# Kernel optimization log

Measured on AMD Instinct MI355X. Metric: run time of the kernel, lower is better.

## Reference

```python
import jax, jax.numpy as jnp
import numpy as np

EPS = 1e-5  # nn.LayerNorm default
H = 16      # n_heads

def _ln(x, s, b):
    m = x.mean(-1, keepdims=True)
    v = x.var(-1, keepdims=True)
    return (x - m) / jnp.sqrt(v + EPS) * s + b


def setup_inputs() -> dict:
    key = jax.random.key(0)
    B, T, D, L, V = 2, 1024, 1024, 6, 32000
    ks = jax.random.split(key, 10)
    def n(k, shape):
        return jax.random.normal(k, shape, dtype=jnp.float32) * 0.02
    return dict(
        x=jax.random.randint(ks[0], (B, T), 0, V),
        tok_emb=n(ks[1], (V, D)),
        pos_emb=n(ks[2], (T, D)),
        Wq=n(ks[3], (L, D, D)), bq=jnp.zeros((L, D), jnp.float32),
        Wk=n(ks[4], (L, D, D)), bk=jnp.zeros((L, D), jnp.float32),
        Wv=n(ks[5], (L, D, D)), bv=jnp.zeros((L, D), jnp.float32),
        ln1_s=jnp.ones((L, D), jnp.float32), ln1_b=jnp.zeros((L, D), jnp.float32),
        W1=n(ks[6], (L, D, 4 * D)), b1=jnp.zeros((L, 4 * D), jnp.float32),
        W2=n(ks[7], (L, 4 * D, D)), b2=jnp.zeros((L, D), jnp.float32),
        ln2_s=jnp.ones((L, D), jnp.float32), ln2_b=jnp.zeros((L, D), jnp.float32),
        Wout=n(ks[8], (D, V)), bout=jnp.zeros((V,), jnp.float32),
    )


def reference(x, tok_emb, pos_emb, Wq, bq, Wk, bk, Wv, bv, ln1_s, ln1_b,
              W1, b1, W2, b2, ln2_s, ln2_b, Wout, bout):
    B, T = x.shape
    D = tok_emb.shape[1]
    hd = D // H
    # embeddings (dropout = identity in eval)
    h = tok_emb[x] + pos_emb[:T]
    # additive causal mask: +1.0 on allowed (tril ones kept), -inf elsewhere,
    # exactly matching torch's tril-ones masked_fill mask
    tril = jnp.tril(jnp.ones((T, T), dtype=h.dtype))
    mask = jnp.where(tril == 0, -jnp.inf, 1.0).astype(h.dtype)
    scale = jnp.asarray(1.0 / np.sqrt(hd), h.dtype)

    def block(h, p):
        wq, bq_, wk, bk_, wv, bv_, l1s, l1b, w1, b1_, w2, b2_, l2s, l2b = p
        def heads(W, b):  # [B,T,D] -> [B,H,T,hd]
            return (h @ W + b).reshape(B, T, H, hd).transpose(0, 2, 1, 3)
        q, k, v = heads(wq, bq_), heads(wk, bk_), heads(wv, bv_)
        s = jnp.einsum('bhqd,bhkd->bhqk', q, k) * scale + mask
        a = jax.nn.softmax(s, axis=-1)
        o = jnp.einsum('bhqk,bhkd->bhqd', a, v).transpose(0, 2, 1, 3).reshape(B, T, D)
        hi = _ln(o + h, l1s, l1b)
        f = jax.nn.relu(hi @ w1 + b1_) @ w2 + b2_
        return _ln(f + hi, l2s, l2b), None

    h, _ = jax.lax.scan(block, h, (Wq, bq, Wk, bk, Wv, bv, ln1_s, ln1_b,
                                   W1, b1, W2, b2, ln2_s, ln2_b))
    return h @ Wout + bout
```

## Files before the change

kernel.cpp:

```cpp
#include <hip/hip_runtime.h>
#include <cstdint>
#include <cstddef>

typedef short bf16x8 __attribute__((ext_vector_type(8)));
typedef float f32x4 __attribute__((ext_vector_type(4)));
typedef unsigned short us4 __attribute__((ext_vector_type(4)));

#define DEV static __device__ __forceinline__

DEV unsigned short f2bf(float f) {
  union { float f; unsigned u; } v; v.f = f;
  unsigned r = v.u + 0x7FFFu + ((v.u >> 16) & 1u);
  return (unsigned short)(r >> 16);
}

DEV void gll16(const void* g, void* l) {
  __builtin_amdgcn_global_load_lds((const __attribute__((address_space(1))) void*)g,
                                   (__attribute__((address_space(3))) void*)l,
                                   16, 0, 0);
}

DEV void embed_body(const int* __restrict__ x, const float* __restrict__ te,
                    const float* __restrict__ pe, float* __restrict__ hf,
                    unsigned short* __restrict__ hb, int row, int tid) {
  int t = row & 1023;
  int tok = x[row];
  float4 v = ((const float4*)(te + (size_t)tok * 1024))[tid];
  float4 p = ((const float4*)(pe + (size_t)t * 1024))[tid];
  v.x += p.x; v.y += p.y; v.z += p.z; v.w += p.w;
  ((float4*)(hf + (size_t)row * 1024))[tid] = v;
  us4 bv; bv[0] = f2bf(v.x); bv[1] = f2bf(v.y); bv[2] = f2bf(v.z); bv[3] = f2bf(v.w);
  ((us4*)(hb + (size_t)row * 1024))[tid] = bv;
}

DEV void wconv_body(const float* __restrict__ W, unsigned short* __restrict__ Wt,
                    int K, int N, int b, float (*tile)[33], int tid) {
  const int nb = N >> 5;
  const int n0 = (b % nb) * 32, k0 = (b / nb) * 32;
  const int tx = tid & 31, ty = tid >> 5;
#pragma unroll
  for (int i = 0; i < 4; ++i)
    tile[ty * 4 + i][tx] = W[(size_t)(k0 + ty * 4 + i) * N + n0 + tx];
  __syncthreads();
#pragma unroll
  for (int i = 0; i < 4; ++i)
    Wt[(size_t)(n0 + ty * 4 + i) * K + k0 + tx] = f2bf(tile[tx][ty * 4 + i]);
}

template <int NP>
DEV void ln_body(const float* __restrict__ a1, const float* __restrict__ res,
                 const float* __restrict__ s, const float* __restrict__ bb,
                 float* __restrict__ out_f, unsigned short* __restrict__ out_b,
                 int row, int tid, float* red) {
  float4 x = ((const float4*)(a1 + (size_t)row * 1024))[tid];
  float4 rv = ((const float4*)(res + (size_t)row * 1024))[tid];
  x.x += rv.x; x.y += rv.y; x.z += rv.z; x.w += rv.w;
#pragma unroll
  for (int pimg = 1; pimg < NP; ++pimg) {
    float4 x2 = ((const float4*)(a1 + (size_t)pimg * 2097152 + (size_t)row * 1024))[tid];
    x.x += x2.x; x.y += x2.y; x.z += x2.z; x.w += x2.w;
  }
  float sum = x.x + x.y + x.z + x.w;
  float sq = x.x * x.x + x.y * x.y + x.z * x.z + x.w * x.w;
#pragma unroll
  for (int mm = 1; mm < 64; mm <<= 1) {
    sum += __shfl_xor(sum, mm, 64);
    sq += __shfl_xor(sq, mm, 64);
  }
  int wid = tid >> 6, lane = tid & 63;
  if (lane == 0) { red[wid] = sum; red[4 + wid] = sq; }
  __syncthreads();
  sum = red[0] + red[1] + red[2] + red[3];
  sq = red[4] + red[5] + red[6] + red[7];
  float mean = sum * (1.f / 1024.f);
  float var = sq * (1.f / 1024.f) - mean * mean;
  float rstd = rsqrtf(var + 1e-5f);
  float4 sv = ((const float4*)s)[tid];
  float4 bv = ((const float4*)bb)[tid];
  float4 y;
  y.x = (x.x - mean) * rstd * sv.x + bv.x;
  y.y = (x.y - mean) * rstd * sv.y + bv.y;
  y.z = (x.z - mean) * rstd * sv.z + bv.z;
  y.w = (x.w - mean) * rstd * sv.w + bv.w;
  ((float4*)(out_f + (size_t)row * 1024))[tid] = y;
  us4 ob; ob[0] = f2bf(y.x); ob[1] = f2bf(y.y); ob[2] = f2bf(y.z); ob[3] = f2bf(y.w);
  ((us4*)(out_b + (size_t)row * 1024))[tid] = ob;
}

DEV void wconv5_select(int bid, const float* Wqf, const float* Wkf,
                       const float* Wvf, const float* W1f, const float* W2f,
                       unsigned short* wsc, float (*tile)[33], int tid) {
  const float* W; unsigned short* Wt; int K, N, b;
  if (bid < 3072) {
    const int sgl = bid >> 10; b = bid & 1023;
    W = sgl == 0 ? Wqf : (sgl == 1 ? Wkf : Wvf);
    Wt = wsc + (size_t)sgl * 1048576; K = 1024; N = 1024;
  } else if (bid < 7168) {
    b = bid - 3072; W = W1f; Wt = wsc + 3145728; K = 1024; N = 4096;
  } else {
    b = bid - 7168; W = W2f; Wt = wsc + 7340032; K = 4096; N = 1024;
  }
  wconv_body(W, Wt, K, N, b, tile, tid);
}

__global__ __launch_bounds__(256) void embed_wconv_kernel(
    const int* __restrict__ x, const float* __restrict__ te,
    const float* __restrict__ pe, float* __restrict__ hf,
    unsigned short* __restrict__ hb,
    const float* __restrict__ Wqf, const float* __restrict__ Wkf,
    const float* __restrict__ Wvf, const float* __restrict__ W1f,
    const float* __restrict__ W2f, unsigned short* __restrict__ wsc) {
  __shared__ float tile[32][33];
  const int bid = blockIdx.x;
  if (bid < 2048) {
    embed_body(x, te, pe, hf, hb, bid, threadIdx.x);
    return;
  }
  wconv5_select(bid - 2048, Wqf, Wkf, Wvf, W1f, W2f, wsc, tile, threadIdx.x);
}

template <int NP>
__global__ __launch_bounds__(256) void ln_wconv5_kernel(
    const float* __restrict__ a1, const float* __restrict__ res,
    const float* __restrict__ s, const float* __restrict__ bb,
    float* __restrict__ out_f, unsigned short* __restrict__ out_b,
    const float* __restrict__ Wqf, const float* __restrict__ Wkf,
    const float* __restrict__ Wvf, const float* __restrict__ W1f,
    const float* __restrict__ W2f, unsigned short* __restrict__ wsc) {
  __shared__ float tile[32][33];
  __shared__ float red[8];
  const int bid = blockIdx.x;
  if (bid < 2048) {
    ln_body<NP>(a1, res, s, bb, out_f, out_b, bid, threadIdx.x, red);
    return;
  }
  wconv5_select(bid - 2048, Wqf, Wkf, Wvf, W1f, W2f, wsc, tile, threadIdx.x);
}

template <int NP>
__global__ __launch_bounds__(256) void ln_add_kernel(
    const float* __restrict__ a1, const float* __restrict__ res,
    const float* __restrict__ s, const float* __restrict__ bb,
    float* __restrict__ out_f, unsigned short* __restrict__ out_b) {
  __shared__ float red[8];
  ln_body<NP>(a1, res, s, bb, out_f, out_b, blockIdx.x, threadIdx.x, red);
}

__global__ __launch_bounds__(256) void wconv_kernel(
    const float* __restrict__ W, unsigned short* __restrict__ Wt, int K, int N) {
  __shared__ float tile[32][33];
  const int nb = N >> 5;
  wconv_body(W, Wt, K, N, blockIdx.y * nb + blockIdx.x, tile, threadIdx.x);
}

template <int BM, int EPI>
__global__ __launch_bounds__(512) void gemm5_kernel(
    const unsigned short* __restrict__ A, const unsigned short* __restrict__ Bt,
    const float* __restrict__ bias1, const float* __restrict__ bias2,
    const float* __restrict__ bias3, void* __restrict__ C1,
    void* __restrict__ C2, void* __restrict__ C3,
    int M, int N, int Kstride, int klen, int nbm) {
  constexpr int BN = 128, BK = 64;
  constexpr int MFR = BM / 64;
  constexpr int AIT = BM / 64;
  __shared__ unsigned short lA[BM * BK];
  __shared__ unsigned short lB[BN * BK];
  const int tid = threadIdx.x;
  const int wid = tid >> 6, lane = tid & 63;
  const int g = lane >> 4, c = lane & 15;
  const int wm = wid >> 1, wn = wid & 1;

  const int nwg = gridDim.x;
  const int q = nwg >> 3, r = nwg & 7;
  const int xcd = blockIdx.x & 7, jj = blockIdx.x >> 3;
  const int wgid = (xcd < r) ? (xcd * (q + 1) + jj)
                             : (r * (q + 1) + (xcd - r) * q + jj);
  const int bm = (wgid % nbm) * BM;
  const int bn = (wgid / nbm) * BN;
  const int k0 = blockIdx.z * klen;

  f32x4 acc[MFR][4];
#pragma unroll
  for (int mi = 0; mi < MFR; ++mi)
#pragma unroll
    for (int ni = 0; ni < 4; ++ni) acc[mi][ni] = f32x4{0.f, 0.f, 0.f, 0.f};

  for (int kb = 0; kb < klen; kb += BK) {
#pragma unroll
    for (int it = 0; it < AIT; ++it) {
      int chunk = it * 512 + tid;
      int row = chunk >> 3, cr = chunk & 7;
      int sc = cr ^ (row & 7);
      gll16(A + (size_t)(bm + row) * Kstride + k0 + kb + sc * 8,
            lA + (size_t)(it * 512 + wid * 64) * 8);
    }
#pragma unroll
    for (int it = 0; it < 2; ++it) {
      int chunk = it * 512 + tid;
      int row = chunk >> 3, cr = chunk & 7;
      int sc = cr ^ (row & 7);
      gll16(Bt + (size_t)(bn + row) * Kstride + k0 + kb + sc * 8,
            lB + (size_t)(it * 512 + wid * 64) * 8);
    }
    __syncthreads();
#pragma unroll
    for (int kk = 0; kk < 2; ++kk) {
      bf16x8 af[MFR], bfr[4];
#pragma unroll
      for (int mi = 0; mi < MFR; ++mi) {
        int row = wm * (BM / 4) + mi * 16 + c;
        int ch = (kk * 4 + g) ^ (row & 7);
        af[mi] = *(const bf16x8*)(lA + row * BK + ch * 8);
      }
#pragma unroll
      for (int ni = 0; ni < 4; ++ni) {
        int row = wn * 64 + ni * 16 + c;
        int ch = (kk * 4 + g) ^ (row & 7);
        bfr[ni] = *(const bf16x8*)(lB + row * BK + ch * 8);
      }
#pragma unroll
      for (int mi = 0; mi < MFR; ++mi)
#pragma unroll
        for (int ni = 0; ni < 4; ++ni)
          acc[mi][ni] = __builtin_amdgcn_mfma_f32_16x16x32_bf16(
              af[mi], bfr[ni], acc[mi][ni], 0, 0, 0);
    }
    __syncthreads();
  }

  const bool z0 = (blockIdx.z == 0);
#pragma unroll
  for (int mi = 0; mi < MFR; ++mi) {
    const int row0 = bm + wm * (BM / 4) + mi * 16 + g * 4;
#pragma unroll
    for (int ni = 0; ni < 4; ++ni) {
      const int col = bn + wn * 64 + ni * 16 + c;
      if constexpr (EPI == 0) {
        float* C = (float*)C1 + (size_t)blockIdx.z * M * N;
        const float bv = z0 ? bias1[col] : 0.f;
#pragma unroll
        for (int rr = 0; rr < 4; ++rr)
          C[(size_t)(row0 + rr) * N + col] = acc[mi][ni][rr] + bv;
      } else if constexpr (EPI == 2) {
        const float bv = bias1[col];
#pragma unroll
        for (int rr = 0; rr < 4; ++rr)
          ((unsigned short*)C1)[(size_t)(row0 + rr) * N + col] =
              f2bf(fmaxf(acc[mi][ni][rr] + bv, 0.f));
      } else {
        if (col < 1024) {
          const float bv = bias1[col];
#pragma unroll
          for (int rr = 0; rr < 4; ++rr)
            ((unsigned short*)C1)[(size_t)(row0 + rr) * 1024 + col] =
                f2bf(acc[mi][ni][rr] + bv);
        } else if (col < 2048) {
          const float bv = bias2[col - 1024];
#pragma unroll
          for (int rr = 0; rr < 4; ++rr)
            ((unsigned short*)C2)[(size_t)(row0 + rr) * 1024 + (col - 1024)] =
                f2bf(acc[mi][ni][rr] + bv);
        } else {
          const int cp = col - 2048;
          const float bv = bias3[cp];
          const int hh = cp >> 6, hd = cp & 63;
#pragma unroll
          for (int rr = 0; rr < 4; ++rr) {
            const int row = row0 + rr;
            const int b = row >> 10, t = row & 1023;
            ((unsigned short*)C3)[(size_t)((b * 16 + hh) * 64 + hd) * 1024 + t] =
                f2bf(acc[mi][ni][rr] + bv);
          }
        }
      }
    }
  }
}

__global__ __launch_bounds__(256) void attn_kernel(
    const unsigned short* __restrict__ q, const unsigned short* __restrict__ k,
    const unsigned short* __restrict__ vt, float* __restrict__ o) {
  __shared__ unsigned short lK[128 * 64];
  __shared__ unsigned short lV[64 * 128];
  __shared__ unsigned short lP[4][16 * 128];
  const int tid = threadIdx.x, wid = tid >> 6, lane = tid & 63;
  const int g = lane >> 4, c = lane & 15;
  const int qb = blockIdx.x * 64;
  const int h = blockIdx.y;
  const int b = blockIdx.z;
  const int qw = qb + wid * 16;

  bf16x8 aq[2];
#pragma unroll
  for (int kk = 0; kk < 2; ++kk)
    aq[kk] = *(const bf16x8*)(q + (size_t)(b * 1024 + qw + c) * 1024 + h * 64 + kk * 32 + g * 8);

  float m_run[4], l_run[4];
  f32x4 acc_o[4];
#pragma unroll
  for (int rr = 0; rr < 4; ++rr) { m_run[rr] = -INFINITY; l_run[rr] = 0.f; }
#pragma unroll
  for (int ni = 0; ni < 4; ++ni) acc_o[ni] = f32x4{0.f, 0.f, 0.f, 0.f};

  const int ntiles = (qb >> 7) + 1;
  for (int kt = 0; kt < ntiles; ++kt) {
#pragma unroll
    for (int it = 0; it < 4; ++it) {
      int chunk = it * 256 + tid;
      int row = chunk >> 3, cr = chunk & 7;
      int sc = cr ^ (row & 7);
      gll16(k + (size_t)(b * 1024 + kt * 128 + row) * 1024 + h * 64 + sc * 8,
            lK + (size_t)(it * 256 + wid * 64) * 8);
    }
#pragma unroll
    for (int it = 0; it < 4; ++it) {
      int chunk = it * 256 + tid;
      int row = chunk >> 4, cr = chunk & 15;
      int sc = cr ^ (row & 7);
      gll16(vt + (size_t)((b * 16 + h) * 64 + row) * 1024 + kt * 128 + sc * 8,
            lV + (size_t)(it * 256 + wid * 64) * 8);
    }
    __syncthreads();

    f32x4 accs[8];
#pragma unroll
    for (int ni = 0; ni < 8; ++ni) accs[ni] = f32x4{0.f, 0.f, 0.f, 0.f};
    __builtin_amdgcn_s_setprio(1);
#pragma unroll
    for (int kk = 0; kk < 2; ++kk)
#pragma unroll
      for (int ni = 0; ni < 8; ++ni) {
        int row = ni * 16 + c;
        int ch = (kk * 4 + g) ^ (row & 7);
        bf16x8 kf = *(const bf16x8*)(lK + row * 64 + ch * 8);
        accs[ni] = __builtin_amdgcn_mfma_f32_16x16x32_bf16(aq[kk], kf, accs[ni], 0, 0, 0);
      }
    __builtin_amdgcn_s_setprio(0);

    const bool diag = (kt == ntiles - 1);
    float p[8][4], rowmax[4];
#pragma unroll
    for (int rr = 0; rr < 4; ++rr) rowmax[rr] = -INFINITY;
#pragma unroll
    for (int ni = 0; ni < 8; ++ni)
#pragma unroll
      for (int rr = 0; rr < 4; ++rr) {
        float s = accs[ni][rr] * 0.125f;
        if (diag) {
          int ktok = kt * 128 + ni * 16 + c;
          int qtok = qw + g * 4 + rr;
          if (ktok > qtok) s = -INFINITY;
        }
        p[ni][rr] = s;
        rowmax[rr] = fmaxf(rowmax[rr], s);
      }
#pragma unroll
    for (int mm = 1; mm < 16; mm <<= 1)
#pragma unroll
      for (int rr = 0; rr < 4; ++rr)
        rowmax[rr] = fmaxf(rowmax[rr], __shfl_xor(rowmax[rr], mm, 64));

    float alpha[4];
#pragma unroll
    for (int rr = 0; rr < 4; ++rr) {
      float mn = fmaxf(m_run[rr], rowmax[rr]);
      alpha[rr] = __expf(m_run[rr] - mn);
      m_run[rr] = mn;
    }
#pragma unroll
    for (int ni = 0; ni < 8; ++ni)
#pragma unroll
      for (int rr = 0; rr < 4; ++rr) p[ni][rr] = __expf(p[ni][rr] - m_run[rr]);

    float rowsum[4];
#pragma unroll
    for (int rr = 0; rr < 4; ++rr)
      rowsum[rr] = ((p[0][rr] + p[1][rr]) + (p[2][rr] + p[3][rr])) +
                   ((p[4][rr] + p[5][rr]) + (p[6][rr] + p[7][rr]));
#pragma unroll
    for (int mm = 1; mm < 16; mm <<= 1)
#pragma unroll
      for (int rr = 0; rr < 4; ++rr) rowsum[rr] += __shfl_xor(rowsum[rr], mm, 64);
#pragma unroll
    for (int rr = 0; rr < 4; ++rr) l_run[rr] = l_run[rr] * alpha[rr] + rowsum[rr];
#pragma unroll
    for (int ni = 0; ni < 4; ++ni)
#pragma unroll
      for (int rr = 0; rr < 4; ++rr) acc_o[ni][rr] *= alpha[rr];

#pragma unroll
    for (int ni = 0; ni < 8; ++ni)
#pragma unroll
      for (int rr = 0; rr < 4; ++rr) {
        int qrow = g * 4 + rr;
        int tok = ni * 16 + c;
        int ch = (tok >> 3) ^ (qrow & 7);
        lP[wid][qrow * 128 + ch * 8 + (tok & 7)] = f2bf(p[ni][rr]);
      }

    __builtin_amdgcn_s_setprio(1);
#pragma unroll
    for (int kk = 0; kk < 4; ++kk) {
      int kc = kk * 4 + g;
      int chp = kc ^ (c & 7);
      bf16x8 pa = *(const bf16x8*)(&lP[wid][c * 128 + chp * 8]);
#pragma unroll
      for (int ni = 0; ni < 4; ++ni) {
        int row = ni * 16 + c;
        int ch = kc ^ (row & 7);
        bf16x8 vf = *(const bf16x8*)(lV + row * 128 + ch * 8);
        acc_o[ni] = __builtin_amdgcn_mfma_f32_16x16x32_bf16(pa, vf, acc_o[ni], 0, 0, 0);
      }
    }
    __builtin_amdgcn_s_setprio(0);
    __syncthreads();
  }

#pragma unroll
  for (int ni = 0; ni < 4; ++ni)
#pragma unroll
    for (int rr = 0; rr < 4; ++rr) {
      int row = b * 1024 + qw + g * 4 + rr;
      int col = h * 64 + ni * 16 + c;
      o[(size_t)row * 1024 + col] = acc_o[ni][rr] / l_run[rr];
    }
}

extern "C" void kernel_launch(void* const* d_in, const int* in_sizes, int n_in,
                              void* d_out, int out_size, void* d_ws, size_t ws_size,
                              hipStream_t stream) {
  const int D = 1024, DFF = 4096, V = 32000, L = 6;
  const int* x = (const int*)d_in[0];
  const float* tok_emb = (const float*)d_in[1];
  const float* pos_emb = (const float*)d_in[2];
  const float* Wq = (const float*)d_in[3];  const float* bq = (const float*)d_in[4];
  const float* Wk = (const float*)d_in[5];  const float* bk = (const float*)d_in[6];
  const float* Wv = (const float*)d_in[7];  const float* bv = (const float*)d_in[8];
  const float* ln1s = (const float*)d_in[9];  const float* ln1b = (const float*)d_in[10];
  const float* W1 = (const float*)d_in[11];  const float* b1 = (const float*)d_in[12];
  const float* W2 = (const float*)d_in[13];  const float* b2 = (const float*)d_in[14];
  const float* ln2s = (const float*)d_in[15]; const float* ln2b = (const float*)d_in[16];
  const float* Wout = (const float*)d_in[17]; const float* bout = (const float*)d_in[18];

  char* ws = (char*)d_ws;
  float* h_res = (float*)(ws + 0);
  float* hi_res = (float*)(ws + 8388608);
  float* tmp = (float*)(ws + 16777216);
  unsigned short* hbf = (unsigned short*)(ws + 25165824);
  unsigned short* qb_ = (unsigned short*)(ws + 29360128);
  unsigned short* kb_ = (unsigned short*)(ws + 33554432);
  unsigned short* vtb = (unsigned short*)(ws + 37748736);
  unsigned short* ffn1 = (unsigned short*)(ws + 41943040);
  unsigned short* wsc = (unsigned short*)(ws + 58720256);
  float* part = (float*)(ws + 58720256 + 25165824);

  embed_wconv_kernel<<<13312, 256, 0, stream>>>(
      x, tok_emb, pos_emb, h_res, hbf,
      Wq, Wk, Wv, W1, W2, wsc);

  for (int l = 0; l < L; ++l) {
    gemm5_kernel<128, 4><<<384, 512, 0, stream>>>(
        hbf, wsc, bq + l * D, bk + l * D, bv + l * D, qb_, kb_, vtb,
        2048, 3072, D, D, 16);
    attn_kernel<<<dim3(16, 16, 2), 256, 0, stream>>>(qb_, kb_, vtb, tmp);
    ln_add_kernel<1><<<2048, 256, 0, stream>>>(
        tmp, h_res, ln1s + l * D, ln1b + l * D, hi_res, hbf);
    gemm5_kernel<256, 2><<<256, 512, 0, stream>>>(
        hbf, wsc + 3145728, b1 + l * DFF, nullptr, nullptr, ffn1, nullptr, nullptr,
        2048, DFF, D, D, 8);
    gemm5_kernel<256, 0><<<dim3(64, 1, 4), 512, 0, stream>>>(
        ffn1, wsc + 7340032, b2 + l * D, nullptr, nullptr, part, nullptr, nullptr,
        2048, D, DFF, 1024, 8);
    if (l < L - 1) {
      ln_wconv5_kernel<4><<<13312, 256, 0, stream>>>(
          part, hi_res, ln2s + l * D, ln2b + l * D, h_res, hbf,
          Wq + (size_t)(l + 1) * D * D, Wk + (size_t)(l + 1) * D * D,
          Wv + (size_t)(l + 1) * D * D, W1 + (size_t)(l + 1) * D * DFF,
          W2 + (size_t)(l + 1) * DFF * D, wsc);
    } else {
      ln_add_kernel<4><<<2048, 256, 0, stream>>>(
          part, hi_res, ln2s + l * D, ln2b + l * D, h_res, hbf);
    }
  }

  wconv_kernel<<<dim3(1000, 32), 256, 0, stream>>>(Wout, wsc, D, V);
  gemm5_kernel<256, 0><<<2000, 512, 0, stream>>>(
      hbf, wsc, bout, nullptr, nullptr, (float*)d_out, nullptr, nullptr,
      2048, V, D, D, 8);
}
```

Baseline: 1.084 ms.

## Add double-buffered FFN1 GEMM and widen attention blocks to 128 queries

Adds a new FFN1 GEMM kernel that double-buffers A and B tiles in LDS, issuing the next K-tile's global-to-LDS loads while MFMAs run on the current tile, with one barrier per iteration. Separately, the attention kernel goes to 512 threads and 128 query rows per block, so each K/V tile loaded into LDS is shared by eight waves instead of four. The GEMM doubles its LDS footprint, which can lower occupancy. The larger attention blocks halve the grid and make causal load imbalance between blocks worse.

```diff
diff --git a/kernel.cpp b/kernel.cpp
--- a/kernel.cpp
+++ b/kernel.cpp
@@ -19,6 +19,8 @@
                                    (__attribute__((address_space(3))) void*)l,
                                    16, 0, 0);
 }
+
+DEV void vm0() { asm volatile("s_waitcnt vmcnt(0)" ::: "memory"); }
 
 DEV void embed_body(const int* __restrict__ x, const float* __restrict__ te,
                     const float* __restrict__ pe, float* __restrict__ hf,
@@ -277,15 +279,114 @@
   }
 }
 
-__global__ __launch_bounds__(256) void attn_kernel(
+template <int EPI>
+__global__ __launch_bounds__(512) void gemm5d_kernel(
+    const unsigned short* __restrict__ A, const unsigned short* __restrict__ Bt,
+    const float* __restrict__ bias1, void* __restrict__ C1,
+    int M, int N, int Kstride, int klen, int nbm) {
+  constexpr int BM = 256, BN = 128, BK = 64;
+  __shared__ unsigned short lA[2][BM * BK];
+  __shared__ unsigned short lB[2][BN * BK];
+  const int tid = threadIdx.x;
+  const int wid = tid >> 6, lane = tid & 63;
+  const int g = lane >> 4, c = lane & 15;
+  const int wm = wid >> 1, wn = wid & 1;
+
+  const int nwg = gridDim.x;
+  const int q = nwg >> 3, r = nwg & 7;
+  const int xcd = blockIdx.x & 7, jj = blockIdx.x >> 3;
+  const int wgid = (xcd < r) ? (xcd * (q + 1) + jj)
+                             : (r * (q + 1) + (xcd - r) * q + jj);
+  const int bm = (wgid % nbm) * BM;
+  const int bn = (wgid / nbm) * BN;
+  const int NT = klen / BK;
+
+  f32x4 acc[4][4];
+#pragma unroll
+  for (int mi = 0; mi < 4; ++mi)
+#pragma unroll
+    for (int ni = 0; ni < 4; ++ni) acc[mi][ni] = f32x4{0.f, 0.f, 0.f, 0.f};
+
+#define STAGE(t_, buf_) do {                                                 \
+    const int kb_ = (t_) * BK;                                               \
+    _Pragma("unroll")                                                        \
+    for (int it = 0; it < 4; ++it) {                                         \
+      int chunk = it * 512 + tid;                                            \
+      int row = chunk >> 3, cr = chunk & 7;                                  \
+      int sc = cr ^ (row & 7);                                               \
+      gll16(A + (size_t)(bm + row) * Kstride + kb_ + sc * 8,                 \
+            lA[buf_] + (size_t)(it * 512 + wid * 64) * 8);                   \
+    }                                                                        \
+    _Pragma("unroll")                                                        \
+    for (int it = 0; it < 2; ++it) {                                         \
+      int chunk = it * 512 + tid;                                            \
+      int row = chunk >> 3, cr = chunk & 7;                                  \
+      int sc = cr ^ (row & 7);                                               \
+      gll16(Bt + (size_t)(bn + row) * Kstride + kb_ + sc * 8,                \
+            lB[buf_] + (size_t)(it * 512 + wid * 64) * 8);                   \
+    } } while (0)
+
+  STAGE(0, 0);
+  vm0();
+  __builtin_amdgcn_s_barrier();
+
+  int cur = 0;
+  for (int t = 0; t < NT; ++t) {
+    if (t + 1 < NT) STAGE(t + 1, cur ^ 1);
+#pragma unroll
+    for (int kk = 0; kk < 2; ++kk) {
+      bf16x8 af[4], bfr[4];
+#pragma unroll
+      for (int mi = 0; mi < 4; ++mi) {
+        int row = wm * 64 + mi * 16 + c;
+        int ch = (kk * 4 + g) ^ (row & 7);
+        af[mi] = *(const bf16x8*)(lA[cur] + row * BK + ch * 8);
+      }
+#pragma unroll
+      for (int ni = 0; ni < 4; ++ni) {
+        int row = wn * 64 + ni * 16 + c;
+        int ch = (kk * 4 + g) ^ (row & 7);
+        bfr[ni] = *(const bf16x8*)(lB[cur] + row * BK + ch * 8);
+      }
+      __builtin_amdgcn_s_setprio(1);
+#pragma unroll
+      for (int mi = 0; mi < 4; ++mi)
+#pragma unroll
+        for (int ni = 0; ni < 4; ++ni)
+          acc[mi][ni] = __builtin_amdgcn_mfma_f32_16x16x32_bf16(
+              af[mi], bfr[ni], acc[mi][ni], 0, 0, 0);
+      __builtin_amdgcn_s_setprio(0);
+    }
+    vm0();
+    __builtin_amdgcn_s_barrier();
+    cur ^= 1;
+  }
+#undef STAGE
+
+#pragma unroll
+  for (int mi = 0; mi < 4; ++mi) {
+    const int row0 = bm + wm * 64 + mi * 16 + g * 4;
+#pragma unroll
+    for (int ni = 0; ni < 4; ++ni) {
+      const int col = bn + wn * 64 + ni * 16 + c;
+      const float bv = bias1[col];
+#pragma unroll
+      for (int rr = 0; rr < 4; ++rr)
+        ((unsigned short*)C1)[(size_t)(row0 + rr) * N + col] =
+            f2bf(fmaxf(acc[mi][ni][rr] + bv, 0.f));
+    }
+  }
+}
+
+__global__ __launch_bounds__(512) void attn_kernel(
     const unsigned short* __restrict__ q, const unsigned short* __restrict__ k,
     const unsigned short* __restrict__ vt, float* __restrict__ o) {
   __shared__ unsigned short lK[128 * 64];
   __shared__ unsigned short lV[64 * 128];
-  __shared__ unsigned short lP[4][16 * 128];
+  __shared__ unsigned short lP[8][16 * 128];
   const int tid = threadIdx.x, wid = tid >> 6, lane = tid & 63;
   const int g = lane >> 4, c = lane & 15;
-  const int qb = blockIdx.x * 64;
+  const int qb = blockIdx.x * 128;
   const int h = blockIdx.y;
   const int b = blockIdx.z;
   const int qw = qb + wid * 16;
@@ -302,23 +403,23 @@
 #pragma unroll
   for (int ni = 0; ni < 4; ++ni) acc_o[ni] = f32x4{0.f, 0.f, 0.f, 0.f};
 
-  const int ntiles = (qb >> 7) + 1;
+  const int ntiles = blockIdx.x + 1;
   for (int kt = 0; kt < ntiles; ++kt) {
 #pragma unroll
-    for (int it = 0; it < 4; ++it) {
-      int chunk = it * 256 + tid;
+    for (int it = 0; it < 2; ++it) {
+      int chunk = it * 512 + tid;
       int row = chunk >> 3, cr = chunk & 7;
       int sc = cr ^ (row & 7);
       gll16(k + (size_t)(b * 1024 + kt * 128 + row) * 1024 + h * 64 + sc * 8,
-            lK + (size_t)(it * 256 + wid * 64) * 8);
-    }
-#pragma unroll
-    for (int it = 0; it < 4; ++it) {
-      int chunk = it * 256 + tid;
+            lK + (size_t)(it * 512 + wid * 64) * 8);
+    }
+#pragma unroll
+    for (int it = 0; it < 2; ++it) {
+      int chunk = it * 512 + tid;
       int row = chunk >> 4, cr = chunk & 15;
       int sc = cr ^ (row & 7);
       gll16(vt + (size_t)((b * 16 + h) * 64 + row) * 1024 + kt * 128 + sc * 8,
-            lV + (size_t)(it * 256 + wid * 64) * 8);
+            lV + (size_t)(it * 512 + wid * 64) * 8);
     }
     __syncthreads();
 
@@ -462,12 +563,11 @@
     gemm5_kernel<128, 4><<<384, 512, 0, stream>>>(
         hbf, wsc, bq + l * D, bk + l * D, bv + l * D, qb_, kb_, vtb,
         2048, 3072, D, D, 16);
-    attn_kernel<<<dim3(16, 16, 2), 256, 0, stream>>>(qb_, kb_, vtb, tmp);
+    attn_kernel<<<dim3(8, 16, 2), 512, 0, stream>>>(qb_, kb_, vtb, tmp);
     ln_add_kernel<1><<<2048, 256, 0, stream>>>(
         tmp, h_res, ln1s + l * D, ln1b + l * D, hi_res, hbf);
-    gemm5_kernel<256, 2><<<256, 512, 0, stream>>>(
-        hbf, wsc + 3145728, b1 + l * DFF, nullptr, nullptr, ffn1, nullptr, nullptr,
-        2048, DFF, D, D, 8);
+    gemm5d_kernel<2><<<256, 512, 0, stream>>>(
+        hbf, wsc + 3145728, b1 + l * DFF, ffn1, 2048, DFF, D, D, 8);
     gemm5_kernel<256, 0><<<dim3(64, 1, 4), 512, 0, stream>>>(
         ffn1, wsc + 7340032, b2 + l * D, nullptr, nullptr, part, nullptr, nullptr,
         2048, D, DFF, 1024, 8);
```

After: 1.095 ms. Within noise of the previous version (+1.0%).

## Use 256x256-tile 1024-thread GEMM for final vocab projection

Applied to the files above, without the earlier changes.

Adds a new GEMM kernel that uses 256x256 output tiles with 16 waves (1024 threads), each wave computing a 64x64 sub-tile with bf16 MFMA. It applies XCD-aware workgroup remapping and swizzled LDS loads through global_load_lds. The final logits projection (2048x32000x1024) now uses this kernel instead of the 256x128 gemm5 variant. The larger tiles raise operand reuse and halve the workgroup count. In exchange the kernel is single-buffered with two barriers per K step, which can expose load latency and lower occupancy.

```diff
diff --git a/kernel.cpp b/kernel.cpp
--- a/kernel.cpp
+++ b/kernel.cpp
@@ -273,6 +273,89 @@
           }
         }
       }
+    }
+  }
+}
+
+__global__ __launch_bounds__(1024) void gemm6_kernel(
+    const unsigned short* __restrict__ A, const unsigned short* __restrict__ Bt,
+    const float* __restrict__ bias1, float* __restrict__ C1,
+    int M, int N, int K, int nbm) {
+  constexpr int BM = 256, BN = 256, BK = 64;
+  __shared__ unsigned short lA[BM * BK];
+  __shared__ unsigned short lB[BN * BK];
+  const int tid = threadIdx.x;
+  const int wid = tid >> 6, lane = tid & 63;
+  const int g = lane >> 4, c = lane & 15;
+  const int wm = wid >> 2, wn = wid & 3;
+
+  const int nwg = gridDim.x;
+  const int q = nwg >> 3, r = nwg & 7;
+  const int xcd = blockIdx.x & 7, jj = blockIdx.x >> 3;
+  const int wgid = (xcd < r) ? (xcd * (q + 1) + jj)
+                             : (r * (q + 1) + (xcd - r) * q + jj);
+  const int bm = (wgid % nbm) * BM;
+  const int bn = (wgid / nbm) * BN;
+
+  f32x4 acc[4][4];
+#pragma unroll
+  for (int mi = 0; mi < 4; ++mi)
+#pragma unroll
+    for (int ni = 0; ni < 4; ++ni) acc[mi][ni] = f32x4{0.f, 0.f, 0.f, 0.f};
+
+  for (int kb = 0; kb < K; kb += BK) {
+#pragma unroll
+    for (int it = 0; it < 2; ++it) {
+      int chunk = it * 1024 + tid;
+      int row = chunk >> 3, cr = chunk & 7;
+      int sc = cr ^ (row & 7);
+      gll16(A + (size_t)(bm + row) * K + kb + sc * 8,
+            lA + (size_t)(it * 1024 + wid * 64) * 8);
+    }
+#pragma unroll
+    for (int it = 0; it < 2; ++it) {
+      int chunk = it * 1024 + tid;
+      int row = chunk >> 3, cr = chunk & 7;
+      int sc = cr ^ (row & 7);
+      gll16(Bt + (size_t)(bn + row) * K + kb + sc * 8,
+            lB + (size_t)(it * 1024 + wid * 64) * 8);
+    }
+    __syncthreads();
+#pragma unroll
+    for (int kk = 0; kk < 2; ++kk) {
+      bf16x8 af[4], bfr[4];
+#pragma unroll
+      for (int mi = 0; mi < 4; ++mi) {
+        int row = wm * 64 + mi * 16 + c;
+        int ch = (kk * 4 + g) ^ (row & 7);
+        af[mi] = *(const bf16x8*)(lA + row * BK + ch * 8);
+      }
+#pragma unroll
+      for (int ni = 0; ni < 4; ++ni) {
+        int row = wn * 64 + ni * 16 + c;
+        int ch = (kk * 4 + g) ^ (row & 7);
+        bfr[ni] = *(const bf16x8*)(lB + row * BK + ch * 8);
+      }
+#pragma unroll
+      for (int mi = 0; mi < 4; ++mi)
+#pragma unroll
+        for (int ni = 0; ni < 4; ++ni)
+          acc[mi][ni] = __builtin_amdgcn_mfma_f32_16x16x32_bf16(
+              af[mi], bfr[ni], acc[mi][ni], 0, 0, 0);
+    }
+    __syncthreads();
+  }
+
+#pragma unroll
+  for (int mi = 0; mi < 4; ++mi) {
+    const int row0 = bm + wm * 64 + mi * 16 + g * 4;
+#pragma unroll
+    for (int ni = 0; ni < 4; ++ni) {
+      const int col = bn + wn * 64 + ni * 16 + c;
+      const float bv = bias1[col];
+#pragma unroll
+      for (int rr = 0; rr < 4; ++rr)
+        C1[(size_t)(row0 + rr) * N + col] = acc[mi][ni][rr] + bv;
     }
   }
 }
@@ -484,7 +567,6 @@
   }
 
   wconv_kernel<<<dim3(1000, 32), 256, 0, stream>>>(Wout, wsc, D, V);
-  gemm5_kernel<256, 0><<<2000, 512, 0, stream>>>(
-      hbf, wsc, bout, nullptr, nullptr, (float*)d_out, nullptr, nullptr,
-      2048, V, D, D, 8);
-}
+  gemm6_kernel<<<1000, 1024, 0, stream>>>(
+      hbf, wsc, bout, (float*)d_out, 2048, V, D, 8);
+}
```

Measured after the change: 1.112 ms. 2.5% more time.
